# Kernel optimization log

Measured on AMD Instinct MI355X. Metric: run time of the kernel, lower is better.

The kernel has to match this reference:

```python
import jax, jax.numpy as jnp
import numpy as np

NEG_INF = -1e9
LRELU_SLOPE = 0.2


def setup_inputs() -> dict:
    N, F_IN, F_OUT = 8192, 256, 128
    key = jax.random.key(0)
    k_adj, k_x, k_w, k_phi = jax.random.split(key, 4)
    adj = (jax.random.uniform(k_adj, (N, N)) < 0.01).astype(jnp.float32)
    x = jax.random.normal(k_x, (N, F_IN), dtype=jnp.float32)
    stdv_w = 1.0 / np.sqrt(F_OUT)
    weight = jax.random.uniform(k_w, (F_IN, F_OUT), minval=-stdv_w, maxval=stdv_w, dtype=jnp.float32)
    bias = jnp.zeros((F_OUT,), dtype=jnp.float32)
    phi = jax.random.uniform(k_phi, (2 * F_OUT, 1), minval=-1.0, maxval=1.0, dtype=jnp.float32)
    return {"adj": adj, "input": x, "weight": weight, "bias": bias, "phi": phi}


def reference(adj, input, weight, bias, phi):
    # x_prime: [N, F_OUT]
    x_prime = input @ weight + bias
    N = adj.shape[0]
    F_out = x_prime.shape[1]
    # S[i, j] = cat(x_i, x_j) @ phi = x_i @ phi[:F] + x_j @ phi[F:]
    # (identical math to the repeat+cat formulation, without the O(N^2*2F) tensor)
    phi_src = phi[:F_out, 0]  # [F_OUT]
    phi_dst = phi[F_out:, 0]  # [F_OUT]
    s_src = x_prime @ phi_src  # [N]
    s_dst = x_prime @ phi_dst  # [N]
    S = s_src[:, None] + s_dst[None, :]  # [N, N]
    S = jnp.where(S >= 0, S, LRELU_SLOPE * S)  # leaky_relu(0.2)
    mask = (adj + jnp.eye(N, dtype=adj.dtype)) > 0
    S_masked = jnp.where(mask, S, NEG_INF)
    attention = jax.nn.softmax(S_masked, axis=1)  # row-wise
    h = attention @ x_prime  # [N, F_OUT]
    return h
```

## Files before the change

### kernel.cpp

```cpp
#include <hip/hip_runtime.h>

#define Nn    8192
#define FIN   256
#define FOUTc 128
#define MAXN  512

__global__ __launch_bounds__(256) void k_prep(const float* __restrict__ w,
                                              const float* __restrict__ phi,
                                              float* __restrict__ wps,
                                              float* __restrict__ wpd)
{
    const int k    = blockIdx.x * 4 + (threadIdx.x >> 6);
    const int lane = threadIdx.x & 63;
    const float2 wv = ((const float2*)(w + (size_t)k * FOUTc))[lane];
    const float2 ps = ((const float2*)phi)[lane];
    const float2 pd = ((const float2*)(phi + FOUTc))[lane];
    float a = wv.x * ps.x + wv.y * ps.y;
    float b = wv.x * pd.x + wv.y * pd.y;
#pragma unroll
    for (int off = 32; off > 0; off >>= 1) {
        a += __shfl_down(a, off, 64);
        b += __shfl_down(b, off, 64);
    }
    if (lane == 0) { wps[k] = a; wpd[k] = b; }
}

__global__ __launch_bounds__(256) void k_s(const float* __restrict__ x,
                                           const float* __restrict__ wps,
                                           const float* __restrict__ wpd,
                                           float* __restrict__ s_src,
                                           float* __restrict__ s_dst)
{
    const int wid = threadIdx.x >> 6, lane = threadIdx.x & 63;
    const int row = blockIdx.x * 4 + wid;
    const float* xr = x + (size_t)row * FIN;
    float a = 0.f, b = 0.f;
#pragma unroll
    for (int q = 0; q < 4; q++) {
        const int k = lane + 64 * q;
        const float xv = xr[k];
        a = fmaf(xv, wps[k], a);
        b = fmaf(xv, wpd[k], b);
    }
#pragma unroll
    for (int off = 32; off > 0; off >>= 1) {
        a += __shfl_down(a, off, 64);
        b += __shfl_down(b, off, 64);
    }
    if (lane == 0) { s_src[row] = a; s_dst[row] = b; }
}

__global__ __launch_bounds__(256) void k_agg(const float* __restrict__ adj,
                                             const float* __restrict__ x,
                                             const float* __restrict__ w,
                                             const float* __restrict__ bias,
                                             const float* __restrict__ s_src,
                                             const float* __restrict__ s_dst,
                                             float* __restrict__ out)
{
    __shared__ int   nbr[MAXN];
    __shared__ float wts[MAXN];
    __shared__ float zs[FIN];
    __shared__ float ph[2][FOUTc];
    __shared__ float red[4];
    __shared__ int   cnt;

    const int tid = threadIdx.x;
    const int i = blockIdx.x;
    if (tid == 0) cnt = 0;
    __syncthreads();

    const float4* arow4 = (const float4*)(adj + (size_t)i * Nn);
    float4 buf[8];
#pragma unroll
    for (int t = 0; t < 8; t++) buf[t] = arow4[t * 256 + tid];

#pragma unroll
    for (int t = 0; t < 8; t++) {
        const int j0 = (t * 256 + tid) * 4;
        const float av[4] = {buf[t].x, buf[t].y, buf[t].z, buf[t].w};
#pragma unroll
        for (int p = 0; p < 4; p++) {
            const int j = j0 + p;
            if (av[p] != 0.f || j == i) {
                const int pos = atomicAdd(&cnt, 1);
                if (pos < MAXN) nbr[pos] = j;
            }
        }
    }
    __syncthreads();
    const int L = (cnt < MAXN) ? cnt : MAXN;

    float lmax = -1e30f;
    for (int n = tid; n < L; n += 256) {
        const float sd = s_dst[nbr[n]];
        wts[n] = sd;
        lmax = fmaxf(lmax, sd);
    }
#pragma unroll
    for (int off = 32; off > 0; off >>= 1) lmax = fmaxf(lmax, __shfl_down(lmax, off, 64));
    if ((tid & 63) == 0) red[tid >> 6] = lmax;
    __syncthreads();
    const float maxd = fmaxf(fmaxf(red[0], red[1]), fmaxf(red[2], red[3]));
    const float ssi = s_src[i];
    const float Sm  = ssi + maxd;
    const float m_i = (Sm >= 0.f) ? Sm : 0.2f * Sm;

    float lsum = 0.f;
    for (int n = tid; n < L; n += 256) {
        float S = ssi + wts[n];
        S = (S >= 0.f) ? S : 0.2f * S;
        const float wv = __expf(S - m_i);
        wts[n] = wv;
        lsum += wv;
    }
#pragma unroll
    for (int off = 32; off > 0; off >>= 1) lsum += __shfl_down(lsum, off, 64);
    __syncthreads();
    if ((tid & 63) == 0) red[tid >> 6] = lsum;
    __syncthreads();
    const float l_i = (red[0] + red[1]) + (red[2] + red[3]);
    const float inv = 1.f / l_i;

    float zc = 0.f;
    for (int n = 0; n < L; n++)
        zc = fmaf(wts[n], x[(size_t)nbr[n] * FIN + tid], zc);
    zs[tid] = zc * inv;
    __syncthreads();

    const int o = tid & 127, half = tid >> 7;
    float acc = 0.f;
    const float* wcol = w + (size_t)(half * 128) * FOUTc + o;
#pragma unroll 8
    for (int k = 0; k < 128; k++)
        acc = fmaf(zs[half * 128 + k], wcol[(size_t)k * FOUTc], acc);
    ph[half][o] = acc;
    __syncthreads();
    if (tid < FOUTc)
        out[(size_t)i * FOUTc + tid] = ph[0][tid] + ph[1][tid] + bias[tid];
}

extern "C" void kernel_launch(void* const* d_in, const int* in_sizes, int n_in,
                              void* d_out, int out_size, void* d_ws, size_t ws_size,
                              hipStream_t stream)
{
    (void)out_size; (void)ws_size;
    const float* adj  = (const float*)d_in[0];
    const float* x    = (const float*)d_in[1];
    const float* w    = (const float*)d_in[2];
    const float* bias = (const float*)d_in[3];
    const float* phi  = (const float*)d_in[4];
    for (int i = 0; i < n_in; i++) {
        switch (in_sizes[i]) {
            case Nn * Nn:     adj  = (const float*)d_in[i]; break;
            case Nn * FIN:    x    = (const float*)d_in[i]; break;
            case FIN * FOUTc: w    = (const float*)d_in[i]; break;
            case FOUTc:       bias = (const float*)d_in[i]; break;
            case 2 * FOUTc:   phi  = (const float*)d_in[i]; break;
        }
    }
    float* out = (float*)d_out;

    float* wps   = (float*)d_ws;
    float* wpd   = wps + FIN;
    float* s_src = wpd + FIN;
    float* s_dst = s_src + Nn;

    hipLaunchKernelGGL(k_prep, dim3(64),   dim3(256), 0, stream, w, phi, wps, wpd);
    hipLaunchKernelGGL(k_s,    dim3(Nn/4), dim3(256), 0, stream, x, wps, wpd, s_src, s_dst);
    hipLaunchKernelGGL(k_agg,  dim3(Nn),   dim3(256), 0, stream,
                       adj, x, w, bias, s_src, s_dst, out);
}
```

Baseline: 418.0 us.

## Precompute x_prime once and aggregate over projected features instead of raw input

Replaces the per-row aggregate-then-project scheme with a tiled GEMM kernel that computes x_prime and both attention scores up front. Aggregation then gathers 128-wide x_prime rows instead of 256-wide raw input rows, and the per-row projection through W is dropped. The adjacency scan is moved into its own kernel that writes neighbour lists to global memory. This trades an extra launch and a global round-trip of neighbour indices for half the gather bandwidth and no per-row matvec.

```diff
diff --git a/kernel.cpp b/kernel.cpp
--- a/kernel.cpp
+++ b/kernel.cpp
@@ -5,66 +5,82 @@
 #define FOUTc 128
 #define MAXN  512
 
-__global__ __launch_bounds__(256) void k_prep(const float* __restrict__ w,
-                                              const float* __restrict__ phi,
-                                              float* __restrict__ wps,
-                                              float* __restrict__ wpd)
-{
-    const int k    = blockIdx.x * 4 + (threadIdx.x >> 6);
-    const int lane = threadIdx.x & 63;
-    const float2 wv = ((const float2*)(w + (size_t)k * FOUTc))[lane];
-    const float2 ps = ((const float2*)phi)[lane];
-    const float2 pd = ((const float2*)(phi + FOUTc))[lane];
-    float a = wv.x * ps.x + wv.y * ps.y;
-    float b = wv.x * pd.x + wv.y * pd.y;
-#pragma unroll
-    for (int off = 32; off > 0; off >>= 1) {
-        a += __shfl_down(a, off, 64);
-        b += __shfl_down(b, off, 64);
-    }
-    if (lane == 0) { wps[k] = a; wpd[k] = b; }
-}
-
-__global__ __launch_bounds__(256) void k_s(const float* __restrict__ x,
-                                           const float* __restrict__ wps,
-                                           const float* __restrict__ wpd,
-                                           float* __restrict__ s_src,
-                                           float* __restrict__ s_dst)
-{
-    const int wid = threadIdx.x >> 6, lane = threadIdx.x & 63;
-    const int row = blockIdx.x * 4 + wid;
-    const float* xr = x + (size_t)row * FIN;
-    float a = 0.f, b = 0.f;
-#pragma unroll
-    for (int q = 0; q < 4; q++) {
-        const int k = lane + 64 * q;
-        const float xv = xr[k];
-        a = fmaf(xv, wps[k], a);
-        b = fmaf(xv, wpd[k], b);
-    }
-#pragma unroll
-    for (int off = 32; off > 0; off >>= 1) {
-        a += __shfl_down(a, off, 64);
-        b += __shfl_down(b, off, 64);
-    }
-    if (lane == 0) { s_src[row] = a; s_dst[row] = b; }
-}
-
-__global__ __launch_bounds__(256) void k_agg(const float* __restrict__ adj,
-                                             const float* __restrict__ x,
-                                             const float* __restrict__ w,
-                                             const float* __restrict__ bias,
-                                             const float* __restrict__ s_src,
-                                             const float* __restrict__ s_dst,
-                                             float* __restrict__ out)
-{
-    __shared__ int   nbr[MAXN];
-    __shared__ float wts[MAXN];
-    __shared__ float zs[FIN];
-    __shared__ float ph[2][FOUTc];
-    __shared__ float red[4];
-    __shared__ int   cnt;
-
+__global__ __launch_bounds__(256) void k_xprime(const float* __restrict__ x,
+                                                const float* __restrict__ w,
+                                                const float* __restrict__ bias,
+                                                const float* __restrict__ phi,
+                                                float* __restrict__ xp,
+                                                float* __restrict__ s_src,
+                                                float* __restrict__ s_dst)
+{
+    __shared__ float Wl[64 * 128];
+    __shared__ float Xl[32][68];
+    __shared__ float Ssum[4][16], Dsum[4][16];
+
+    const int tid = threadIdx.x;
+    const int c = tid & 127, g = tid >> 7;
+    const int wv_ = tid >> 6, lane = tid & 63;
+    const int row0 = blockIdx.x * 32;
+
+    float acc[16];
+    const float bv = bias[c];
+#pragma unroll
+    for (int r = 0; r < 16; r++) acc[r] = bv;
+
+    for (int ko = 0; ko < FIN; ko += 64) {
+#pragma unroll
+        for (int t = 0; t < 8; t++) {
+            const int idx = t * 1024 + tid * 4;
+            *(float4*)&Wl[idx] = *(const float4*)&w[(size_t)ko * FOUTc + idx];
+        }
+#pragma unroll
+        for (int t = 0; t < 2; t++) {
+            const int idx = t * 1024 + tid * 4;
+            const int r = idx >> 6, k = idx & 63;
+            const float4 v = *(const float4*)&x[(size_t)(row0 + r) * FIN + ko + k];
+            Xl[r][k] = v.x; Xl[r][k + 1] = v.y; Xl[r][k + 2] = v.z; Xl[r][k + 3] = v.w;
+        }
+        __syncthreads();
+        for (int k = 0; k < 64; k++) {
+            const float wvv = Wl[k * FOUTc + c];
+#pragma unroll
+            for (int r = 0; r < 16; r++)
+                acc[r] = fmaf(Xl[g * 16 + r][k], wvv, acc[r]);
+        }
+        __syncthreads();
+    }
+
+#pragma unroll
+    for (int r = 0; r < 16; r++)
+        xp[(size_t)(row0 + g * 16 + r) * FOUTc + c] = acc[r];
+
+    const float phs = phi[c], phd = phi[FOUTc + c];
+#pragma unroll
+    for (int r = 0; r < 16; r++) {
+        float ps = acc[r] * phs;
+        float pd = acc[r] * phd;
+#pragma unroll
+        for (int off = 32; off > 0; off >>= 1) {
+            ps += __shfl_down(ps, off, 64);
+            pd += __shfl_down(pd, off, 64);
+        }
+        if (lane == 0) { Ssum[wv_][r] = ps; Dsum[wv_][r] = pd; }
+    }
+    __syncthreads();
+    if (tid < 32) {
+        const int g2 = tid >> 4, r = tid & 15;
+        const int row = row0 + g2 * 16 + r;
+        s_src[row] = Ssum[2 * g2][r] + Ssum[2 * g2 + 1][r];
+        s_dst[row] = Dsum[2 * g2][r] + Dsum[2 * g2 + 1][r];
+    }
+}
+
+__global__ __launch_bounds__(256) void k_scan(const float* __restrict__ adj,
+                                              int* __restrict__ g_cnt,
+                                              int* __restrict__ g_nbr)
+{
+    __shared__ int nbr[MAXN];
+    __shared__ int cnt;
     const int tid = threadIdx.x;
     const int i = blockIdx.x;
     if (tid == 0) cnt = 0;
@@ -90,10 +106,32 @@
     }
     __syncthreads();
     const int L = (cnt < MAXN) ? cnt : MAXN;
+    if (tid == 0) g_cnt[i] = L;
+    for (int n = tid; n < L; n += 256)
+        g_nbr[(size_t)i * MAXN + n] = nbr[n];
+}
+
+__global__ __launch_bounds__(256) void k_soft(const int* __restrict__ g_cnt,
+                                              const int* __restrict__ g_nbr,
+                                              const float* __restrict__ s_src,
+                                              const float* __restrict__ s_dst,
+                                              const float* __restrict__ xp,
+                                              float* __restrict__ out)
+{
+    __shared__ int   js[MAXN];
+    __shared__ float wts[MAXN];
+    __shared__ float ph[2][FOUTc];
+    __shared__ float red[4];
+
+    const int tid = threadIdx.x;
+    const int i = blockIdx.x;
+    const int L = g_cnt[i];
 
     float lmax = -1e30f;
     for (int n = tid; n < L; n += 256) {
-        const float sd = s_dst[nbr[n]];
+        const int j = g_nbr[(size_t)i * MAXN + n];
+        js[n] = j;
+        const float sd = s_dst[j];
         wts[n] = sd;
         lmax = fmaxf(lmax, sd);
     }
@@ -119,25 +157,16 @@
     __syncthreads();
     if ((tid & 63) == 0) red[tid >> 6] = lsum;
     __syncthreads();
-    const float l_i = (red[0] + red[1]) + (red[2] + red[3]);
-    const float inv = 1.f / l_i;
-
-    float zc = 0.f;
-    for (int n = 0; n < L; n++)
-        zc = fmaf(wts[n], x[(size_t)nbr[n] * FIN + tid], zc);
-    zs[tid] = zc * inv;
-    __syncthreads();
-
-    const int o = tid & 127, half = tid >> 7;
-    float acc = 0.f;
-    const float* wcol = w + (size_t)(half * 128) * FOUTc + o;
-#pragma unroll 8
-    for (int k = 0; k < 128; k++)
-        acc = fmaf(zs[half * 128 + k], wcol[(size_t)k * FOUTc], acc);
-    ph[half][o] = acc;
+    const float inv = 1.f / ((red[0] + red[1]) + (red[2] + red[3]));
+
+    const int c = tid & 127, half = tid >> 7;
+    float h = 0.f;
+    for (int n = half; n < L; n += 2)
+        h = fmaf(wts[n], xp[(size_t)js[n] * FOUTc + c], h);
+    ph[half][c] = h;
     __syncthreads();
     if (tid < FOUTc)
-        out[(size_t)i * FOUTc + tid] = ph[0][tid] + ph[1][tid] + bias[tid];
+        out[(size_t)i * FOUTc + tid] = (ph[0][tid] + ph[1][tid]) * inv;
 }
 
 extern "C" void kernel_launch(void* const* d_in, const int* in_sizes, int n_in,
@@ -161,13 +190,16 @@
     }
     float* out = (float*)d_out;
 
-    float* wps   = (float*)d_ws;
-    float* wpd   = wps + FIN;
-    float* s_src = wpd + FIN;
+    char* ws = (char*)d_ws;
+    float* xp    = (float*)ws;
+    float* s_src = (float*)(ws + (size_t)Nn * FOUTc * 4);
     float* s_dst = s_src + Nn;
-
-    hipLaunchKernelGGL(k_prep, dim3(64),   dim3(256), 0, stream, w, phi, wps, wpd);
-    hipLaunchKernelGGL(k_s,    dim3(Nn/4), dim3(256), 0, stream, x, wps, wpd, s_src, s_dst);
-    hipLaunchKernelGGL(k_agg,  dim3(Nn),   dim3(256), 0, stream,
-                       adj, x, w, bias, s_src, s_dst, out);
-}
+    int*   g_cnt = (int*)(s_dst + Nn);
+    int*   g_nbr = g_cnt + Nn;
+
+    hipLaunchKernelGGL(k_xprime, dim3(Nn / 32), dim3(256), 0, stream,
+                       x, w, bias, phi, xp, s_src, s_dst);
+    hipLaunchKernelGGL(k_scan,   dim3(Nn),      dim3(256), 0, stream, adj, g_cnt, g_nbr);
+    hipLaunchKernelGGL(k_soft,   dim3(Nn),      dim3(256), 0, stream,
+                       g_cnt, g_nbr, s_src, s_dst, xp, out);
+}
```

Result: slower. 454.1 us (+8.6%).
